# Optimization experiments

Hardware: AMD Instinct MI355X
Metric: run time of the kernel (lower is better)

## Reference

```python
import jax, jax.numpy as jnp
import numpy as np

TAU = 1.0
EPS = 1e-8
JITTER = 1e-6
W_OCC, W_ENT, W_COLLAPSE = 1.0, 0.0, 0.1


def fps_anchors_mu(mu, mask_bool, K):
    """Farthest-point sampling of K anchors from mu [B,N,3], mask_bool [B,N]."""
    B, N, _ = mu.shape
    barange = jnp.arange(B)
    cnt = jnp.maximum(mask_bool.sum(1, keepdims=True), 1)  # [B,1]
    mean = (mu * mask_bool[..., None]).sum(1, keepdims=True) / cnt[..., None]
    d2 = ((mu - mean) ** 2).sum(-1)
    d2 = jnp.where(mask_bool, d2, -1.0)
    first = jnp.argmax(d2, axis=-1)  # [B]
    last = mu[barange, first]  # [B,3]
    min_d2 = ((mu - last[:, None, :]) ** 2).sum(-1)
    min_d2 = jnp.where(mask_bool, min_d2, -1.0)

    def step(md2, _):
        sel = jnp.argmax(md2, axis=-1)  # [B]
        lm = mu[barange, sel]  # [B,3]
        nd2 = ((mu - lm[:, None, :]) ** 2).sum(-1)
        nd2 = jnp.where(mask_bool, nd2, -1.0)
        md2 = jnp.where(md2 == -1.0, nd2, jnp.minimum(md2, nd2))
        return md2, sel

    _, sels = jax.lax.scan(step, min_d2, None, length=K - 1)  # sels [K-1,B]
    idx = jnp.concatenate([first[:, None], sels.T], axis=1)  # [B,K]
    return jax.lax.stop_gradient(idx)


def merge_gaussians_soft(mu, Sigma, A):
    denom = jnp.maximum(A.sum(axis=1, keepdims=True), EPS)  # [B,1,K]
    w = A / denom  # [B,N,K]
    mu_c = jnp.einsum('bnk,bnd->bkd', w, mu)  # [B,K,3]
    intra = jnp.einsum('bnk,bnij->bkij', w, Sigma)  # [B,K,3,3]
    diff = mu[:, :, None, :] - mu_c[:, None, :, :]  # [B,N,K,3]
    inter = jnp.einsum('bnk,bnkd,bnke->bkde', w, diff, diff)
    Sigma_c = intra + inter
    Sigma_c = 0.5 * (Sigma_c + jnp.swapaxes(Sigma_c, -1, -2))
    Sigma_c = Sigma_c + JITTER * jnp.eye(3, dtype=Sigma_c.dtype)
    return mu_c, Sigma_c


def collapse_loss(A, mask):
    B, N, K = A.shape
    Am = A * mask[..., None]
    X = jnp.swapaxes(Am, 1, 2)  # [B,K,N]
    X = X / jnp.maximum(jnp.linalg.norm(X, axis=-1, keepdims=True), EPS)
    G = jnp.einsum('bkn,bln->bkl', X, X)
    eye = jnp.eye(K, dtype=A.dtype)[None]
    off = (G - eye) * (1.0 - eye)
    return jnp.mean(off ** 2)


def reference(s, mu, Sigma, mask, W_proj, slot_embed, log_sigma_mu, w_sem, w_mu):
    B, N, C = s.shape
    K = slot_embed.shape[0]
    mask_bool = mask > 0.5

    # semantic logits
    s_proj = jnp.einsum('bnc,dc->bnd', s, W_proj)  # Linear, no bias
    logits_sem = jnp.einsum('bnc,kc->bnk', s_proj, slot_embed) / max(TAU, 1e-6)

    # spatial logits from FPS anchors
    idx = fps_anchors_mu(mu, mask_bool, K)  # [B,K]
    mu_anchor = jnp.take_along_axis(mu, idx[..., None], axis=1)  # [B,K,3]
    dist2 = ((mu[:, :, None, :] - mu_anchor[:, None, :, :]) ** 2).sum(-1)  # [B,N,K]
    sigma2 = jnp.maximum(jnp.exp(log_sigma_mu), 1e-4) ** 2
    logits_mu = -dist2 / (2.0 * sigma2)

    logits = w_sem * logits_sem + w_mu * logits_mu
    logits = jnp.where(mask[..., None] < 0.5, -1e9, logits)
    A = jax.nn.softmax(logits, axis=-1) * mask[..., None]

    denom = jnp.maximum(A.sum(axis=1), 1e-8)  # [B,K]
    s_c = jnp.einsum('bnk,bnc->bkc', A, s) / denom[..., None]
    mu_c, Sigma_c = merge_gaussians_soft(mu, Sigma, A)

    # losses
    occ = A.sum(axis=1)
    occ = occ / jnp.maximum(occ.sum(axis=-1, keepdims=True), 1e-8)
    target = jnp.full_like(occ, 1.0 / max(K, 1))
    loss_occ = jnp.mean((occ - target) ** 2)
    Ac = jnp.maximum(A, 1e-8)
    ent = -(Ac * jnp.log(Ac)).sum(-1)
    ent = (ent * mask).sum() / jnp.maximum(mask.sum(), 1.0)
    loss_collapse = collapse_loss(A, mask)
    total = W_OCC * loss_occ + W_ENT * ent + W_COLLAPSE * loss_collapse
    return A, s_c, mu_c, Sigma_c, total


def setup_inputs() -> dict:
    key = jax.random.key(0)
    ks = jax.random.split(key, 8)
    B, N, C, K = 4, 8192, 128, 683
    s = jax.random.normal(ks[0], (B, N, C), dtype=jnp.float32)
    mu = jax.random.normal(ks[1], (B, N, 3), dtype=jnp.float32)
    Sig = jax.random.normal(ks[2], (B, N, 3, 3), dtype=jnp.float32)
    Sigma = 0.5 * (Sig + jnp.swapaxes(Sig, -1, -2))
    mask = jnp.ones((B, N), dtype=jnp.float32)
    W_proj = jax.random.normal(ks[3], (C, C), dtype=jnp.float32) / np.sqrt(C)
    slot_embed = jax.random.normal(ks[4], (K, C), dtype=jnp.float32) * 0.02
    log_sigma_mu = jnp.zeros((), dtype=jnp.float32)  # sigma_mu_init = 1.0
    w_sem = jnp.ones((), dtype=jnp.float32)
    w_mu = jnp.ones((), dtype=jnp.float32)
    return {"s": s, "mu": mu, "Sigma": Sigma, "mask": mask, "W_proj": W_proj,
            "slot_embed": slot_embed, "log_sigma_mu": log_sigma_mu,
            "w_sem": w_sem, "w_mu": w_mu}
```

## Files before the change

### kernel.cpp

```cpp
#include <hip/hip_runtime.h>
#include <hip/hip_bf16.h>
#include <math.h>

#define B_ 4
#define N_ 8192
#define C_ 128
#define K_ 683
#define KP_ 768
#define KT_ 704

#define WS_ET      0
#define WS_ANCH    98304
#define WS_EXT     110592
#define WS_EPART   634880
#define WS_MPART   1355776
#define WS_SUMA    2142208
#define WS_NORM    2145024
#define WS_LOSSP2  2147840
#define WS_ST      2147968
#define WS_AT      4245120
#define WS_NEW_END 16828032
#define OLD_PART   634880
#define OLD_SUMA   4419584
#define OLD_NORM   4422400
#define OLD_GPART  4425216
#define OLD_LOSSP  9143808

#define OUT_A      0
#define OUT_SC     22380544ULL
#define OUT_MUC    22730240ULL
#define OUT_SGC    22738436ULL
#define OUT_TOT    22763024ULL

typedef __attribute__((ext_vector_type(8))) short bf16x8s;
typedef __attribute__((ext_vector_type(4))) float f32x4;

static __device__ __forceinline__ unsigned short f2bf_rne(float f) {
  unsigned int u = __builtin_bit_cast(unsigned int, f);
  unsigned int r = (u + 0x7fffu + ((u >> 16) & 1u)) >> 16;
  return (unsigned short)r;
}

static __device__ __forceinline__ unsigned int f2ord(float f) {
  unsigned int u = __builtin_bit_cast(unsigned int, f);
  return (u & 0x80000000u) ? ~u : (u | 0x80000000u);
}

static __device__ __forceinline__ unsigned long long umax64(unsigned long long a,
                                                           unsigned long long b) {
  return a > b ? a : b;
}

__global__ __launch_bounds__(256) void build_ET_k(const float* __restrict__ Wp,
                                                  const float* __restrict__ se,
                                                  float* __restrict__ ET) {
  int idx = blockIdx.x * 256 + threadIdx.x;
  if (idx >= C_ * KP_) return;
  int c = idx / KP_;
  int k = idx % KP_;
  float acc = 0.f;
  if (k < K_) {
    for (int d = 0; d < C_; d++) acc = fmaf(se[k * C_ + d], Wp[d * C_ + c], acc);
  }
  ET[idx] = acc;
}

__global__ __launch_bounds__(512, 1) void fused_k(const float* __restrict__ s,
    const float* __restrict__ mu, const float* __restrict__ Sigma,
    const float* __restrict__ mask, const float* __restrict__ ET,
    float* __restrict__ anchors, float* __restrict__ ext,
    float* __restrict__ A, unsigned short* __restrict__ sT) {
  const int bid = blockIdx.x;
  const int tid = threadIdx.x;

  __shared__ __align__(16) float s_lds[32][132];
  __shared__ __align__(16) float et_lds[8][KP_];
  __shared__ __align__(16) float muL[N_ * 3];
  __shared__ __align__(16) float Tt[64][72];
  __shared__ double redd[8][4];
  __shared__ unsigned long long redk[2][8];
  __shared__ float an_s[4];

  if (bid >= 1092) {
    const int sb = bid - 1092;
    const int b = sb >> 6;
    const int rest = sb & 63;
    const int chalf = rest >> 5;
    const int ns = rest & 31;
    const int c0 = chalf * 64, n0 = ns * 256;
#pragma unroll
    for (int t2 = 0; t2 < 4; t2++) {
      const int nb = n0 + t2 * 64;
      {
        int n_loc = tid >> 3;
        int cb = (tid & 7) * 8;
        const float* sp = s + ((size_t)(b * N_ + nb + n_loc)) * C_ + c0 + cb;
        float4 v0 = *(const float4*)(sp);
        float4 v1 = *(const float4*)(sp + 4);
        Tt[cb + 0][n_loc] = v0.x; Tt[cb + 1][n_loc] = v0.y;
        Tt[cb + 2][n_loc] = v0.z; Tt[cb + 3][n_loc] = v0.w;
        Tt[cb + 4][n_loc] = v1.x; Tt[cb + 5][n_loc] = v1.y;
        Tt[cb + 6][n_loc] = v1.z; Tt[cb + 7][n_loc] = v1.w;
      }
      __syncthreads();
      {
        int row = tid >> 3;
        int qo = tid & 7;
        float4 f0 = *(const float4*)(&Tt[row][qo * 8]);
        float4 f1 = *(const float4*)(&Tt[row][qo * 8 + 4]);
        unsigned short o[8];
        o[0] = f2bf_rne(f0.x); o[1] = f2bf_rne(f0.y); o[2] = f2bf_rne(f0.z); o[3] = f2bf_rne(f0.w);
        o[4] = f2bf_rne(f1.x); o[5] = f2bf_rne(f1.y); o[6] = f2bf_rne(f1.z); o[7] = f2bf_rne(f1.w);
        unsigned short* dst = sT + ((size_t)(b * C_ + c0 + row)) * N_ + nb + qo * 8;
        *(uint4*)dst = *(uint4*)o;
      }
      __syncthreads();
    }
    return;
  }

  if (bid >= 1028) {
    int idx = (bid - 1028) * 512 + tid;
    if (idx < B_ * N_) {
      float x = mu[(size_t)idx * 3 + 0];
      float y = mu[(size_t)idx * 3 + 1];
      float z = mu[(size_t)idx * 3 + 2];
      const float* S = Sigma + (size_t)idx * 9;
      float* e = ext + (size_t)idx * 16;
      e[0] = x; e[1] = y; e[2] = z;
      e[3] = x * x; e[4] = x * y; e[5] = x * z;
      e[6] = y * y; e[7] = y * z; e[8] = z * z;
      e[9] = S[0]; e[10] = S[1]; e[11] = S[2]; e[12] = S[4]; e[13] = S[5]; e[14] = S[8];
      e[15] = 1.f;
    }
    return;
  }

  if (bid >= 4) {
    const int gb = bid - 4;
    const int b = gb >> 8;
    const int n0 = (gb & 255) * 32;
    const int nt = tid >> 6;
    const int kt = tid & 63;
    {
      const float* sb = s + ((size_t)(b * N_ + n0)) * C_;
      int r = tid >> 4;
      int cb = (tid & 15) * 8;
#pragma unroll
      for (int q = 0; q < 2; q++) {
        float4 v = *(const float4*)(sb + (size_t)r * C_ + cb + q * 4);
        *(float4*)(&s_lds[r][cb + q * 4]) = v;
      }
    }
    float acc[4][12];
#pragma unroll
    for (int i = 0; i < 4; i++)
#pragma unroll
      for (int j = 0; j < 12; j++) acc[i][j] = 0.f;

    for (int cc = 0; cc < 16; cc++) {
      __syncthreads();
#pragma unroll
      for (int q = 0; q < 3; q++) {
        int fid = q * 512 + tid;
        int cl = fid / 192;
        int o4 = fid % 192;
        *(float4*)(&et_lds[cl][o4 * 4]) = *(const float4*)(ET + (size_t)(cc * 8 + cl) * KP_ + o4 * 4);
      }
      __syncthreads();
#pragma unroll
      for (int c8 = 0; c8 < 8; c8++) {
        int c = cc * 8 + c8;
        float sv0 = s_lds[nt * 4 + 0][c];
        float sv1 = s_lds[nt * 4 + 1][c];
        float sv2 = s_lds[nt * 4 + 2][c];
        float sv3 = s_lds[nt * 4 + 3][c];
#pragma unroll
        for (int j = 0; j < 12; j++) {
          float ev = et_lds[c8][kt + 64 * j];
          acc[0][j] = fmaf(sv0, ev, acc[0][j]);
          acc[1][j] = fmaf(sv1, ev, acc[1][j]);
          acc[2][j] = fmaf(sv2, ev, acc[2][j]);
          acc[3][j] = fmaf(sv3, ev, acc[3][j]);
        }
      }
    }
#pragma unroll
    for (int i = 0; i < 4; i++) {
      float* Arow = A + ((size_t)(b * N_ + n0 + nt * 4 + i)) * K_;
#pragma unroll
      for (int j = 0; j < 12; j++) {
        int k = kt + 64 * j;
        if (k < K_) Arow[k] = acc[i][j];
      }
    }
    return;
  }

  const int b = bid;
  const int t = tid;
  const int wv = t >> 6;
  const float* mub = mu + (size_t)b * N_ * 3;
  const float* mkb = mask + (size_t)b * N_;
  float px[16], py[16], pz[16], md[16];

  double sx = 0, sy = 0, sz = 0, sc = 0;
#pragma unroll
  for (int i = 0; i < 16; i++) {
    int p = i * 512 + t;
    px[i] = mub[p * 3 + 0];
    py[i] = mub[p * 3 + 1];
    pz[i] = mub[p * 3 + 2];
    muL[p * 3 + 0] = px[i];
    muL[p * 3 + 1] = py[i];
    muL[p * 3 + 2] = pz[i];
    float mk = mkb[p];
    bool valid = (mk > 0.5f);
    md[i] = valid ? 3.4e38f : -1.f;
    if (valid) { sx += px[i]; sy += py[i]; sz += pz[i]; sc += 1.0; }
  }
  for (int off = 32; off; off >>= 1) {
    sx += __shfl_xor(sx, off);
    sy += __shfl_xor(sy, off);
    sz += __shfl_xor(sz, off);
    sc += __shfl_xor(sc, off);
  }
  if ((t & 63) == 0) { redd[wv][0] = sx; redd[wv][1] = sy; redd[wv][2] = sz; redd[wv][3] = sc; }
  __syncthreads();
  if (t == 0) {
    double ax0 = 0, ay0 = 0, az0 = 0, ac = 0;
    for (int w = 0; w < 8; w++) { ax0 += redd[w][0]; ay0 += redd[w][1]; az0 += redd[w][2]; ac += redd[w][3]; }
    if (ac < 1.0) ac = 1.0;
    an_s[0] = (float)(ax0 / ac); an_s[1] = (float)(ay0 / ac); an_s[2] = (float)(az0 / ac);
  }
  __syncthreads();

  float ax, ay, az;
  {
    float cx = an_s[0], cy = an_s[1], cz = an_s[2];
    float bv = -2.f, bv2 = -2.f;
    int bi = 0, bi2 = 0;
#pragma unroll
    for (int i = 0; i < 16; i++) {
      float dx = px[i] - cx, dy = py[i] - cy, dz = pz[i] - cz;
      float d2 = __fadd_rn(__fadd_rn(__fmul_rn(dx, dx), __fmul_rn(dy, dy)), __fmul_rn(dz, dz));
      float v = (md[i] < 0.f) ? -1.f : d2;
      int p = i * 512 + t;
      if (i & 1) { if (v > bv2) { bv2 = v; bi2 = p; } }
      else       { if (v > bv)  { bv = v;  bi = p; } }
    }
    if (bv2 > bv || (bv2 == bv && bi2 < bi)) { bv = bv2; bi = bi2; }
    unsigned long long k0 = ((unsigned long long)f2ord(bv) << 32) | (unsigned int)(~bi);
    for (int off = 32; off; off >>= 1) {
      unsigned long long ok = __shfl_xor(k0, off);
      if (ok > k0) k0 = ok;
    }
    if ((t & 63) == 0) redk[0][wv] = k0;
    __syncthreads();
    unsigned long long a0 = redk[0][0], a1 = redk[0][1], a2 = redk[0][2], a3 = redk[0][3];
    unsigned long long a4 = redk[0][4], a5 = redk[0][5], a6 = redk[0][6], a7 = redk[0][7];
    unsigned long long bk = umax64(umax64(umax64(a0, a1), umax64(a2, a3)),
                                  umax64(umax64(a4, a5), umax64(a6, a7)));
    int besti = (int)(~(unsigned int)bk);
    ax = muL[besti * 3 + 0]; ay = muL[besti * 3 + 1]; az = muL[besti * 3 + 2];
    if (t == 0) {
      float aa = ax * ax + ay * ay + az * az;
      float4 st = {ax, ay, az, aa};
      *(float4*)(anchors + ((size_t)b * KP_ + 0) * 4) = st;
    }
  }

  for (int k = 1; k < K_; k++) {
    const int par = k & 1;
    float bv = -2.f, bv2 = -2.f;
    int bi = 0, bi2 = 0;
#pragma unroll
    for (int i = 0; i < 16; i++) {
      float dx = px[i] - ax, dy = py[i] - ay, dz = pz[i] - az;
      float d2 = __fadd_rn(__fadd_rn(__fmul_rn(dx, dx), __fmul_rn(dy, dy)), __fmul_rn(dz, dz));
      float m = fminf(md[i], d2);
      md[i] = m;
      int p = i * 512 + t;
      if (i & 1) { if (m > bv2) { bv2 = m; bi2 = p; } }
      else       { if (m > bv)  { bv = m;  bi = p; } }
    }
    if (bv2 > bv || (bv2 == bv && bi2 < bi)) { bv = bv2; bi = bi2; }
    unsigned long long kk = ((unsigned long long)f2ord(bv) << 32) | (unsigned int)(~bi);
    for (int off = 32; off; off >>= 1) {
      unsigned long long ok = __shfl_xor(kk, off);
      if (ok > kk) kk = ok;
    }
    if ((t & 63) == 0) redk[par][wv] = kk;
    __syncthreads();
    unsigned long long a0 = redk[par][0], a1 = redk[par][1], a2 = redk[par][2], a3 = redk[par][3];
    unsigned long long a4 = redk[par][4], a5 = redk[par][5], a6 = redk[par][6], a7 = redk[par][7];
    unsigned long long bk = umax64(umax64(umax64(a0, a1), umax64(a2, a3)),
                                  umax64(umax64(a4, a5), umax64(a6, a7)));
    int besti = (int)(~(unsigned int)bk);
    ax = muL[besti * 3 + 0]; ay = muL[besti * 3 + 1]; az = muL[besti * 3 + 2];
    if (t == 0) {
      float aa = ax * ax + ay * ay + az * az;
      float4 st = {ax, ay, az, aa};
      *(float4*)(anchors + ((size_t)b * KP_ + k) * 4) = st;
    }
  }
  for (int k = K_ + t; k < KP_; k += 512) {
    float4 z4 = {0.f, 0.f, 0.f, 0.f};
    *(float4*)(anchors + ((size_t)b * KP_ + k) * 4) = z4;
  }
}

__global__ __launch_bounds__(256) void spatial_softmax_k(
    const float* __restrict__ mu, const float* __restrict__ mask,
    const float* __restrict__ anchors, const float* __restrict__ lsm_p,
    const float* __restrict__ wsem_p, const float* __restrict__ wmu_p,
    float* __restrict__ A) {
  const int bid = blockIdx.x;
  const int b = bid >> 11;
  const int n0 = (bid & 2047) * 4;
  const int tid = threadIdx.x;
  const int wv = tid >> 6;
  const int lane = tid & 63;
  __shared__ __align__(16) float anch_lds[KP_][4];
  for (int q = tid; q < KP_; q += 256)
    *(float4*)(&anch_lds[q][0]) = *(const float4*)(anchors + ((size_t)b * KP_ + q) * 4);
  __syncthreads();

  const float sg = fmaxf(expf(lsm_p[0]), 1e-4f);
  const float inv2s2 = 0.5f / (sg * sg);
  const float wsem = wsem_p[0];
  const float wmu = wmu_p[0];

  const size_t gr = (size_t)b * N_ + n0 + wv;
  const float* mp = mu + gr * 3;
  float x = mp[0], y = mp[1], z = mp[2];
  float mq = x * x + y * y + z * z;
  float mk = mask[gr];
  float* Arow = A + gr * K_;

  float v[11];
  float m = -3e38f;
#pragma unroll
  for (int j = 0; j < 11; j++) {
    int k = lane + 64 * j;
    if (k < K_) {
      float lsem = Arow[k];
      float4 a4 = *(const float4*)(&anch_lds[k][0]);
      float tdot = x * a4.x + y * a4.y + z * a4.z;
      float d2 = mq - 2.f * tdot + a4.w;
      float l = wsem * lsem - wmu * d2 * inv2s2;
      if (mk < 0.5f) l = -1e9f;
      v[j] = l;
    } else v[j] = -1e30f;
    m = fmaxf(m, v[j]);
  }
  for (int off = 32; off; off >>= 1) m = fmaxf(m, __shfl_xor(m, off));
  float sum = 0.f;
#pragma unroll
  for (int j = 0; j < 11; j++) { float e = expf(v[j] - m); v[j] = e; sum += e; }
  for (int off = 32; off; off >>= 1) sum += __shfl_xor(sum, off);
  float r = mk / sum;
#pragma unroll
  for (int j = 0; j < 11; j++) {
    int k = lane + 64 * j;
    if (k < K_) Arow[k] = v[j] * r;
  }
}

__global__ __launch_bounds__(256) void transpose_at_k(const float* __restrict__ A,
    unsigned short* __restrict__ At) {
  const int bid = blockIdx.x;
  const int ntile = bid % 128;
  const int rem = bid / 128;
  const int kt = rem % 12;
  const int b = rem / 12;
  const int k0 = kt * 64, n0 = ntile * 64;
  const int tid = threadIdx.x;
  __shared__ __align__(16) unsigned short T[64][72];

  {
    const int n_loc = tid >> 4;
    const int k4 = (tid & 15) * 4;
#pragma unroll
    for (int nn = 0; nn < 4; nn++) {
      int n = n_loc + 16 * nn;
      const float* ar = A + ((size_t)(b * N_ + n0 + n)) * K_;
#pragma unroll
      for (int q = 0; q < 4; q++) {
        int kk = k0 + k4 + q;
        float f = (kk < K_) ? ar[kk] : 0.f;
        T[k4 + q][n] = f2bf_rne(f);
      }
    }
  }
  __syncthreads();
  {
    const int k_loc = tid >> 2;
    const int c = tid & 3;
    uint4 v0 = *(const uint4*)(&T[k_loc][c * 16]);
    uint4 v1 = *(const uint4*)(&T[k_loc][c * 16 + 8]);
    unsigned short* dst = At + ((size_t)(b * KP_ + k0 + k_loc)) * N_ + n0 + c * 16;
    *(uint4*)dst = v0;
    *(uint4*)(dst + 8) = v1;
  }
}

__global__ __launch_bounds__(256) void gemm2_mfma_k(const unsigned short* __restrict__ At,
    const unsigned short* __restrict__ sT, float* __restrict__ mpart) {
  const int bid = blockIdx.x;
  const int np = bid / 24;
  const int rem = bid % 24;
  const int b = rem / 6;
  const int kt2 = rem % 6;
  const int k0 = kt2 * 128;
  const int tid = threadIdx.x;
  const int l = tid & 63;
  const int w = tid >> 6;
  const int wr = w >> 1, wc = w & 1;

  __shared__ __align__(16) unsigned short Ak_lds[128 * 72];
  __shared__ __align__(16) unsigned short Bc_lds[128 * 72];

  f32x4 acc[4][4];
#pragma unroll
  for (int i = 0; i < 4; i++)
#pragma unroll
    for (int j = 0; j < 4; j++) acc[i][j] = (f32x4){0.f, 0.f, 0.f, 0.f};

  const unsigned short* gk = At + ((size_t)(b * KP_ + k0)) * N_;
  const unsigned short* gc = sT + ((size_t)(b * C_)) * N_;
  const int nbase = np * 4096;

  for (int ch = 0; ch < 64; ch++) {
    const int n0 = nbase + ch * 64;
    __syncthreads();
#pragma unroll
    for (int q = 0; q < 4; q++) {
      int chunk = tid + 256 * q;
      int row = chunk >> 3, slot = chunk & 7;
      uint4 v = *(const uint4*)(gk + (size_t)row * N_ + n0 + slot * 8);
      *(uint4*)(Ak_lds + row * 72 + slot * 8) = v;
      uint4 v2 = *(const uint4*)(gc + (size_t)row * N_ + n0 + slot * 8);
      *(uint4*)(Bc_lds + row * 72 + slot * 8) = v2;
    }
    __syncthreads();
#pragma unroll
    for (int ks = 0; ks < 2; ks++) {
      const int noff = (l >> 4) * 8 + ks * 32;
      bf16x8s af[4], bfr[4];
#pragma unroll
      for (int f = 0; f < 4; f++) {
        af[f]  = *(const bf16x8s*)(Ak_lds + (wr * 64 + f * 16 + (l & 15)) * 72 + noff);
        bfr[f] = *(const bf16x8s*)(Bc_lds + (wc * 64 + f * 16 + (l & 15)) * 72 + noff);
      }
#pragma unroll
      for (int i = 0; i < 4; i++)
#pragma unroll
        for (int j = 0; j < 4; j++)
          acc[i][j] = __builtin_amdgcn_mfma_f32_16x16x32_bf16(af[i], bfr[j], acc[i][j], 0, 0, 0);
    }
  }
  float* mp = mpart + ((size_t)((np * 4 + b) * KP_ + k0)) * C_;
#pragma unroll
  for (int i = 0; i < 4; i++) {
#pragma unroll
    for (int j = 0; j < 4; j++) {
#pragma unroll
      for (int r = 0; r < 4; r++) {
        int ki = wr * 64 + i * 16 + (l >> 4) * 4 + r;
        int ci = wc * 64 + j * 16 + (l & 15);
        mp[(size_t)ki * C_ + ci] = acc[i][j][r];
      }
    }
  }
}

__global__ __launch_bounds__(256) void gemm2_ext_k(const float* __restrict__ A,
    const float* __restrict__ ext, float* __restrict__ epart) {
  const int bid = blockIdx.x;
  const int np = bid / 44;
  const int rem = bid % 44;
  const int b = rem / 11;
  const int k0 = (rem % 11) * 64;
  const int n0 = np * 1024;
  const int tid = threadIdx.x;
  const int kt = tid & 15;
  const int ft = tid >> 4;
  __shared__ __align__(16) float A_lds[32][64];
  __shared__ __align__(16) float F_lds[32][32];
  float acc[4][2];
#pragma unroll
  for (int c = 0; c < 4; c++) { acc[c][0] = 0.f; acc[c][1] = 0.f; }
  float asq[4] = {0.f, 0.f, 0.f, 0.f};

  for (int ch = 0; ch < 32; ch++) {
    int nb = n0 + ch * 32;
    __syncthreads();
#pragma unroll
    for (int p = 0; p < 8; p++) {
      int q = tid + 256 * p; int r = q >> 6; int c = q & 63; int k = k0 + c;
      A_lds[r][c] = (k < K_) ? A[((size_t)(b * N_ + nb + r)) * K_ + k] : 0.f;
    }
#pragma unroll
    for (int p = 0; p < 2; p++) {
      int q = tid + 256 * p; int r = q >> 4; int e = q & 15;
      F_lds[r][e] = ext[((size_t)(b * N_ + nb + r)) * 16 + e];
      F_lds[r][16 + e] = 0.f;
    }
    __syncthreads();
#pragma unroll
    for (int i = 0; i < 32; i++) {
      float a0 = A_lds[i][kt * 4 + 0];
      float a1 = A_lds[i][kt * 4 + 1];
      float a2 = A_lds[i][kt * 4 + 2];
      float a3 = A_lds[i][kt * 4 + 3];
      if (ft == 0) {
        asq[0] = fmaf(a0, a0, asq[0]); asq[1] = fmaf(a1, a1, asq[1]);
        asq[2] = fmaf(a2, a2, asq[2]); asq[3] = fmaf(a3, a3, asq[3]);
      }
#pragma unroll
      for (int f = 0; f < 2; f++) {
        float fv = F_lds[i][ft * 2 + f];
        acc[0][f] = fmaf(a0, fv, acc[0][f]);
        acc[1][f] = fmaf(a1, fv, acc[1][f]);
        acc[2][f] = fmaf(a2, fv, acc[2][f]);
        acc[3][f] = fmaf(a3, fv, acc[3][f]);
      }
    }
  }
#pragma unroll
  for (int c = 0; c < 4; c++) {
    size_t base = ((size_t)((np * 4 + b) * KT_ + k0 + kt * 4 + c)) * 32;
#pragma unroll
    for (int f = 0; f < 2; f++) {
      int fidx = ft * 2 + f;
      if (fidx < 16) epart[base + fidx] = acc[c][f];
    }
    if (ft == 0) epart[base + 16] = asq[c];
  }
}

__global__ __launch_bounds__(256) void postproc2_k(const float* __restrict__ mpart,
    const float* __restrict__ epart, float* __restrict__ out,
    float* __restrict__ sumA_ws, float* __restrict__ norm_ws) {
  const int gw = blockIdx.x * 4 + (threadIdx.x >> 6);
  const int lane = threadIdx.x & 63;
  const int b = gw / K_;
  const int k = gw % K_;
  float v0 = 0.f, v1 = 0.f, v2 = 0.f, v3 = 0.f;
#pragma unroll
  for (int np = 0; np < 2; np++) {
    const float* r = mpart + ((size_t)((np * 4 + b) * KP_ + k)) * C_;
    v0 += r[lane];
    v1 += r[64 + lane];
  }
#pragma unroll
  for (int np = 0; np < 8; np++) {
    const float* e = epart + ((size_t)((np * 4 + b) * KT_ + k)) * 32;
    if (lane < 16) v2 += e[lane];
    if (lane == 0) v3 += e[16];
  }
  float sumA = __shfl(v2, 15);
  float asq = __shfl(v3, 0);
  float denom = fmaxf(sumA, 1e-8f);
  float inv = 1.f / denom;
  out[OUT_SC + ((size_t)(b * K_ + k)) * C_ + lane] = v0 * inv;
  out[OUT_SC + ((size_t)(b * K_ + k)) * C_ + 64 + lane] = v1 * inv;
  float m0 = __shfl(v2, 0) * inv;
  float m1 = __shfl(v2, 1) * inv;
  float m2 = __shfl(v2, 2) * inv;
  if (lane < 3) out[OUT_MUC + ((size_t)(b * K_ + k)) * 3 + lane] = (lane == 0) ? m0 : ((lane == 1) ? m1 : m2);
  float W = sumA * inv;
  float fac = 2.f - W;
  float M2s[6], Sgs[6];
#pragma unroll
  for (int j = 0; j < 6; j++) { M2s[j] = __shfl(v2, 3 + j); Sgs[j] = __shfl(v2, 9 + j); }
  if (lane < 9) {
    int d = lane / 3, e = lane % 3;
    int lo = min(d, e), hi = max(d, e);
    int j = hi + 2 * lo - ((lo * (lo - 1)) >> 1);
    float mud = (d == 0) ? m0 : ((d == 1) ? m1 : m2);
    float mue = (e == 0) ? m0 : ((e == 1) ? m1 : m2);
    float M2j = (j == 0) ? M2s[0] : (j == 1) ? M2s[1] : (j == 2) ? M2s[2] : (j == 3) ? M2s[3] : (j == 4) ? M2s[4] : M2s[5];
    float Sgj = (j == 0) ? Sgs[0] : (j == 1) ? Sgs[1] : (j == 2) ? Sgs[2] : (j == 3) ? Sgs[3] : (j == 4) ? Sgs[4] : Sgs[5];
    float val = (Sgj + M2j) * inv - mud * mue * fac;
    if (d == e) val += 1e-6f;
    out[OUT_SGC + ((size_t)(b * K_ + k)) * 9 + lane] = val;
  }
  if (lane == 0) { sumA_ws[b * KT_ + k] = sumA; norm_ws[b * KT_ + k] = sqrtf(asq); }
}

__global__ __launch_bounds__(256) void gram_mfma_k(const unsigned short* __restrict__ At,
    const float* __restrict__ norm_ws, float* __restrict__ lossp) {
  const int bid = blockIdx.x;
  const int b = bid / 21;
  int p = bid % 21;
  int tk = 0, tl = 0;
  { int pp = p; for (int r0 = 0; r0 < 6; r0++) { int cnt = 6 - r0; if (pp < cnt) { tk = r0; tl = r0 + pp; break; } pp -= cnt; } }
  const int k0 = tk * 128, l0 = tl * 128;
  const int tid = threadIdx.x;
  const int l = tid & 63;
  const int w = tid >> 6;
  const int wr = w >> 1, wc = w & 1;

  __shared__ __align__(16) unsigned short Ak_lds[128 * 72];
  __shared__ __align__(16) unsigned short Al_lds[128 * 72];
  __shared__ float nk_s[128], nl_s[128], red_s[4];

  if (tid < 128) {
    int kk = k0 + tid;
    nk_s[tid] = (kk < K_) ? fmaxf(norm_ws[b * KT_ + kk], 1e-8f) : 1.f;
  } else {
    int ll2 = l0 + tid - 128;
    nl_s[tid - 128] = (ll2 < K_) ? fmaxf(norm_ws[b * KT_ + ll2], 1e-8f) : 1.f;
  }

  f32x4 acc[4][4];
#pragma unroll
  for (int i = 0; i < 4; i++)
#pragma unroll
    for (int j = 0; j < 4; j++) acc[i][j] = (f32x4){0.f, 0.f, 0.f, 0.f};

  const unsigned short* gk = At + ((size_t)(b * KP_ + k0)) * N_;
  const unsigned short* gl = At + ((size_t)(b * KP_ + l0)) * N_;

  for (int ch = 0; ch < 128; ch++) {
    const int n0 = ch * 64;
    __syncthreads();
#pragma unroll
    for (int q = 0; q < 4; q++) {
      int chunk = tid + 256 * q;
      int row = chunk >> 3, slot = chunk & 7;
      uint4 v = *(const uint4*)(gk + (size_t)row * N_ + n0 + slot * 8);
      *(uint4*)(Ak_lds + row * 72 + slot * 8) = v;
      uint4 v2 = *(const uint4*)(gl + (size_t)row * N_ + n0 + slot * 8);
      *(uint4*)(Al_lds + row * 72 + slot * 8) = v2;
    }
    __syncthreads();
#pragma unroll
    for (int ks = 0; ks < 2; ks++) {
      const int noff = (l >> 4) * 8 + ks * 32;
      bf16x8s af[4], bfr[4];
#pragma unroll
      for (int f = 0; f < 4; f++) {
        af[f]  = *(const bf16x8s*)(Ak_lds + (wr * 64 + f * 16 + (l & 15)) * 72 + noff);
        bfr[f] = *(const bf16x8s*)(Al_lds + (wc * 64 + f * 16 + (l & 15)) * 72 + noff);
      }
#pragma unroll
      for (int i = 0; i < 4; i++)
#pragma unroll
        for (int j = 0; j < 4; j++)
          acc[i][j] = __builtin_amdgcn_mfma_f32_16x16x32_bf16(af[i], bfr[j], acc[i][j], 0, 0, 0);
    }
  }

  float local = 0.f;
  const float wgt = (tk == tl) ? 1.f : 2.f;
#pragma unroll
  for (int i = 0; i < 4; i++) {
#pragma unroll
    for (int j = 0; j < 4; j++) {
#pragma unroll
      for (int r = 0; r < 4; r++) {
        int ki = wr * 64 + i * 16 + (l >> 4) * 4 + r;
        int li = wc * 64 + j * 16 + (l & 15);
        int gkk = k0 + ki, gll = l0 + li;
        if (gkk < K_ && gll < K_ && gkk != gll) {
          float g = acc[i][j][r];
          float x = g / (nk_s[ki] * nl_s[li]);
          local = fmaf(wgt * x, x, local);
        }
      }
    }
  }
  for (int off = 32; off; off >>= 1) local += __shfl_xor(local, off);
  if ((tid & 63) == 0) red_s[w] = local;
  __syncthreads();
  if (tid == 0) lossp[bid] = red_s[0] + red_s[1] + red_s[2] + red_s[3];
}

__global__ __launch_bounds__(256) void final2_k(const float* __restrict__ sumA_ws,
    const float* __restrict__ lossp, float* __restrict__ out) {
  const int lane = threadIdx.x & 63;
  const int wv = threadIdx.x >> 6;
  __shared__ float occ_s[4];
  __shared__ float col_s[4];
  float sb = 0.f;
  for (int k = lane; k < K_; k += 64) sb += sumA_ws[wv * KT_ + k];
  for (int off = 32; off; off >>= 1) sb += __shfl_xor(sb, off);
  float Sb = fmaxf(sb, 1e-8f);
  float lo = 0.f;
  const float tgt = 1.f / (float)K_;
  for (int k = lane; k < K_; k += 64) {
    float o = sumA_ws[wv * KT_ + k] / Sb - tgt;
    lo = fmaf(o, o, lo);
  }
  for (int off = 32; off; off >>= 1) lo += __shfl_xor(lo, off);
  if (lane == 0) occ_s[wv] = lo;
  float c = 0.f;
  for (int i = threadIdx.x; i < 84; i += 256) c += lossp[i];
  for (int off = 32; off; off >>= 1) c += __shfl_xor(c, off);
  if (lane == 0) col_s[wv] = c;
  __syncthreads();
  if (threadIdx.x == 0) {
    float loss_occ = (occ_s[0] + occ_s[1] + occ_s[2] + occ_s[3]) / (float)(B_ * K_);
    float coll = (col_s[0] + col_s[1] + col_s[2] + col_s[3]) / ((float)B_ * K_ * K_);
    out[OUT_TOT] = loss_occ + 0.1f * coll;
  }
}

__global__ __launch_bounds__(256) void gemm2_k(const float* __restrict__ A,
    const float* __restrict__ s, const float* __restrict__ ext,
    float* __restrict__ part) {
  const int bid = blockIdx.x;
  const int np = bid / 44;
  const int rem = bid % 44;
  const int b = rem / 11;
  const int k0 = (rem % 11) * 64;
  const int n0 = np * 1024;
  const int tid = threadIdx.x;
  const int kt = tid & 15;
  const int ft = tid >> 4;
  __shared__ __align__(16) float A_lds[32][64];
  __shared__ __align__(16) float F_lds[32][160];
  float acc[4][10];
#pragma unroll
  for (int c = 0; c < 4; c++)
#pragma unroll
    for (int f = 0; f < 10; f++) acc[c][f] = 0.f;
  float asq[4] = {0.f, 0.f, 0.f, 0.f};
  for (int ch = 0; ch < 32; ch++) {
    int nb = n0 + ch * 32;
    __syncthreads();
#pragma unroll
    for (int p = 0; p < 8; p++) {
      int q = tid + 256 * p; int r = q >> 6; int c = q & 63; int k = k0 + c;
      A_lds[r][c] = (k < K_) ? A[((size_t)(b * N_ + nb + r)) * K_ + k] : 0.f;
    }
#pragma unroll
    for (int p = 0; p < 16; p++) {
      int q = tid + 256 * p; int r = q >> 7; int c = q & 127;
      F_lds[r][c] = s[((size_t)(b * N_ + nb + r)) * C_ + c];
    }
#pragma unroll
    for (int p = 0; p < 2; p++) {
      int q = tid + 256 * p; int r = q >> 4; int e = q & 15;
      F_lds[r][128 + e] = ext[((size_t)(b * N_ + nb + r)) * 16 + e];
      F_lds[r][144 + e] = 0.f;
    }
    __syncthreads();
#pragma unroll
    for (int i = 0; i < 32; i++) {
      float a0 = A_lds[i][kt * 4 + 0];
      float a1 = A_lds[i][kt * 4 + 1];
      float a2 = A_lds[i][kt * 4 + 2];
      float a3 = A_lds[i][kt * 4 + 3];
      if (ft == 0) {
        asq[0] = fmaf(a0, a0, asq[0]); asq[1] = fmaf(a1, a1, asq[1]);
        asq[2] = fmaf(a2, a2, asq[2]); asq[3] = fmaf(a3, a3, asq[3]);
      }
#pragma unroll
      for (int f = 0; f < 10; f++) {
        float fv = F_lds[i][ft * 10 + f];
        acc[0][f] = fmaf(a0, fv, acc[0][f]);
        acc[1][f] = fmaf(a1, fv, acc[1][f]);
        acc[2][f] = fmaf(a2, fv, acc[2][f]);
        acc[3][f] = fmaf(a3, fv, acc[3][f]);
      }
    }
  }
#pragma unroll
  for (int c = 0; c < 4; c++) {
    size_t base = ((size_t)((np * 4 + b) * KT_ + k0 + kt * 4 + c)) * 168;
#pragma unroll
    for (int f = 0; f < 10; f++) part[base + ft * 10 + f] = acc[c][f];
    if (ft == 0) part[base + 160] = asq[c];
  }
}

__global__ __launch_bounds__(256) void postproc_k(const float* __restrict__ part,
    float* __restrict__ out, float* __restrict__ sumA_ws, float* __restrict__ norm_ws) {
  const int gw = blockIdx.x * 4 + (threadIdx.x >> 6);
  const int lane = threadIdx.x & 63;
  const int b = gw / K_;
  const int k = gw % K_;
  float v0 = 0.f, v1 = 0.f, v2 = 0.f, v3 = 0.f;
  for (int np = 0; np < 8; np++) {
    const float* r = part + ((size_t)((np * 4 + b) * KT_ + k)) * 168;
    v0 += r[lane];
    v1 += r[64 + lane];
    if (lane < 16) v2 += r[128 + lane];
    if (lane == 0) v3 += r[160];
  }
  float sumA = __shfl(v2, 15);
  float asq = __shfl(v3, 0);
  float denom = fmaxf(sumA, 1e-8f);
  float inv = 1.f / denom;
  out[OUT_SC + ((size_t)(b * K_ + k)) * C_ + lane] = v0 * inv;
  out[OUT_SC + ((size_t)(b * K_ + k)) * C_ + 64 + lane] = v1 * inv;
  float m0 = __shfl(v2, 0) * inv;
  float m1 = __shfl(v2, 1) * inv;
  float m2 = __shfl(v2, 2) * inv;
  if (lane < 3) out[OUT_MUC + ((size_t)(b * K_ + k)) * 3 + lane] = (lane == 0) ? m0 : ((lane == 1) ? m1 : m2);
  float W = sumA * inv;
  float fac = 2.f - W;
  float M2s[6], Sgs[6];
#pragma unroll
  for (int j = 0; j < 6; j++) { M2s[j] = __shfl(v2, 3 + j); Sgs[j] = __shfl(v2, 9 + j); }
  if (lane < 9) {
    int d = lane / 3, e = lane % 3;
    int lo = min(d, e), hi = max(d, e);
    int j = hi + 2 * lo - ((lo * (lo - 1)) >> 1);
    float mud = (d == 0) ? m0 : ((d == 1) ? m1 : m2);
    float mue = (e == 0) ? m0 : ((e == 1) ? m1 : m2);
    float M2j = (j == 0) ? M2s[0] : (j == 1) ? M2s[1] : (j == 2) ? M2s[2] : (j == 3) ? M2s[3] : (j == 4) ? M2s[4] : M2s[5];
    float Sgj = (j == 0) ? Sgs[0] : (j == 1) ? Sgs[1] : (j == 2) ? Sgs[2] : (j == 3) ? Sgs[3] : (j == 4) ? Sgs[4] : Sgs[5];
    float val = (Sgj + M2j) * inv - mud * mue * fac;
    if (d == e) val += 1e-6f;
    out[OUT_SGC + ((size_t)(b * K_ + k)) * 9 + lane] = val;
  }
  if (lane == 0) { sumA_ws[b * KT_ + k] = sumA; norm_ws[b * KT_ + k] = sqrtf(asq); }
}

__device__ __forceinline__ int swz(int f) { return f ^ (((f >> 5) & 3) << 3); }

__global__ __launch_bounds__(256) void gram_k(const float* __restrict__ A,
                                              float* __restrict__ Gpart) {
  const int bid = blockIdx.x;
  const int np = bid & 1;
  int q = bid >> 1;
  const int b = q / 21;
  int p = q % 21;
  int tk = 0, tl = 0;
  { int pp = p; for (int r0 = 0; r0 < 6; r0++) { int cnt = 6 - r0; if (pp < cnt) { tk = r0; tl = r0 + pp; break; } pp -= cnt; } }
  const int k0 = tk * 128, l0 = tl * 128;
  const int n0 = np * 4096;
  const int tid = threadIdx.x;
  const int ktid = tid & 15, ltid = tid >> 4;
  const bool diag = (tk == tl);
  __shared__ __align__(16) float Ak[32][128];
  __shared__ __align__(16) float Al[32][128];
  float acc[8][8];
#pragma unroll
  for (int i = 0; i < 8; i++)
#pragma unroll
    for (int j = 0; j < 8; j++) acc[i][j] = 0.f;
  const int kb = swz(ktid * 8);
  const int lb = swz(ltid * 8);
  for (int ch = 0; ch < 128; ch++) {
    int nb = n0 + ch * 32;
    __syncthreads();
#pragma unroll
    for (int pq = 0; pq < 16; pq++) {
      int qq = tid + 256 * pq; int r = qq >> 7; int c = qq & 127;
      int kk = k0 + c;
      Ak[r][swz(c)] = (kk < K_) ? A[((size_t)(b * N_ + nb + r)) * K_ + kk] : 0.f;
      if (!diag) {
        int ll = l0 + c;
        Al[r][swz(c)] = (ll < K_) ? A[((size_t)(b * N_ + nb + r)) * K_ + ll] : 0.f;
      }
    }
    __syncthreads();
    const float (*Alp)[128] = diag ? Ak : Al;
#pragma unroll
    for (int i = 0; i < 32; i++) {
      float4 ka = *(const float4*)(&Ak[i][kb]);
      float4 kb4 = *(const float4*)(&Ak[i][kb + 4]);
      float4 la = *(const float4*)(&Alp[i][lb]);
      float4 lb4 = *(const float4*)(&Alp[i][lb + 4]);
      float av[8] = {ka.x, ka.y, ka.z, ka.w, kb4.x, kb4.y, kb4.z, kb4.w};
      float lv[8] = {la.x, la.y, la.z, la.w, lb4.x, lb4.y, lb4.z, lb4.w};
#pragma unroll
      for (int ii = 0; ii < 8; ii++)
#pragma unroll
        for (int jj = 0; jj < 8; jj++)
          acc[ii][jj] = fmaf(av[ii], lv[jj], acc[ii][jj]);
    }
  }
#pragma unroll
  for (int ii = 0; ii < 8; ii++) {
    int kk = k0 + ktid * 8 + ii;
    float* gp = Gpart + ((size_t)((np * 4 + b) * KP_ + kk)) * KP_ + l0 + ltid * 8;
#pragma unroll
    for (int jj = 0; jj < 8; jj++) gp[jj] = acc[ii][jj];
  }
}

__global__ __launch_bounds__(256) void loss_part_k(const float* __restrict__ Gpart,
    const float* __restrict__ norm_ws, float* __restrict__ lossp) {
  const long long total = (long long)B_ * 21 * 16384;
  float local = 0.f;
  for (long long idx = (long long)blockIdx.x * 256 + threadIdx.x; idx < total; idx += (long long)512 * 256) {
    int e = (int)(idx & 16383);
    int rest = (int)(idx >> 14);
    int p = rest % 21;
    int b = rest / 21;
    int tk = 0, tl = 0;
    { int pp = p; for (int r0 = 0; r0 < 6; r0++) { int cnt = 6 - r0; if (pp < cnt) { tk = r0; tl = r0 + pp; break; } pp -= cnt; } }
    int i = e >> 7, j = e & 127;
    int k = tk * 128 + i, l = tl * 128 + j;
    if (k < K_ && l < K_ && k != l) {
      size_t i0 = ((size_t)((0 * 4 + b) * KP_ + k)) * KP_ + l;
      size_t i1 = ((size_t)((1 * 4 + b) * KP_ + k)) * KP_ + l;
      float g = Gpart[i0] + Gpart[i1];
      float nk = fmaxf(norm_ws[b * KT_ + k], 1e-8f);
      float nl2 = fmaxf(norm_ws[b * KT_ + l], 1e-8f);
      float x = g / (nk * nl2);
      float wgt = (tk == tl) ? 1.f : 2.f;
      local = fmaf(wgt * x, x, local);
    }
  }
  __shared__ float red[4];
  for (int off = 32; off; off >>= 1) local += __shfl_xor(local, off);
  if ((threadIdx.x & 63) == 0) red[threadIdx.x >> 6] = local;
  __syncthreads();
  if (threadIdx.x == 0) lossp[blockIdx.x] = red[0] + red[1] + red[2] + red[3];
}

__global__ __launch_bounds__(256) void final_k(const float* __restrict__ sumA_ws,
    const float* __restrict__ lossp, float* __restrict__ out) {
  const int lane = threadIdx.x & 63;
  const int wv = threadIdx.x >> 6;
  __shared__ float occ_s[4];
  __shared__ float col_s[4];
  float sb = 0.f;
  for (int k = lane; k < K_; k += 64) sb += sumA_ws[wv * KT_ + k];
  for (int off = 32; off; off >>= 1) sb += __shfl_xor(sb, off);
  float Sb = fmaxf(sb, 1e-8f);
  float lo = 0.f;
  const float tgt = 1.f / (float)K_;
  for (int k = lane; k < K_; k += 64) {
    float o = sumA_ws[wv * KT_ + k] / Sb - tgt;
    lo = fmaf(o, o, lo);
  }
  for (int off = 32; off; off >>= 1) lo += __shfl_xor(lo, off);
  if (lane == 0) occ_s[wv] = lo;
  float c = lossp[threadIdx.x] + lossp[threadIdx.x + 256];
  for (int off = 32; off; off >>= 1) c += __shfl_xor(c, off);
  if (lane == 0) col_s[wv] = c;
  __syncthreads();
  if (threadIdx.x == 0) {
    float loss_occ = (occ_s[0] + occ_s[1] + occ_s[2] + occ_s[3]) / (float)(B_ * K_);
    float coll = (col_s[0] + col_s[1] + col_s[2] + col_s[3]) / ((float)B_ * K_ * K_);
    out[OUT_TOT] = loss_occ + 0.1f * coll;
  }
}

extern "C" void kernel_launch(void* const* d_in, const int* in_sizes, int n_in,
                              void* d_out, int out_size, void* d_ws, size_t ws_size,
                              hipStream_t stream) {
  const float* s = (const float*)d_in[0];
  const float* mu = (const float*)d_in[1];
  const float* Sigma = (const float*)d_in[2];
  const float* mask = (const float*)d_in[3];
  const float* Wp = (const float*)d_in[4];
  const float* se = (const float*)d_in[5];
  const float* lsm = (const float*)d_in[6];
  const float* wsem = (const float*)d_in[7];
  const float* wmu = (const float*)d_in[8];
  float* out = (float*)d_out;
  float* ws = (float*)d_ws;

  float* ET = ws + WS_ET;
  float* anch = ws + WS_ANCH;
  float* ext = ws + WS_EXT;

  const bool use_mfma = ws_size >= (size_t)WS_NEW_END * 4;

  if (use_mfma) {
    float* epart = ws + WS_EPART;
    float* mpart = ws + WS_MPART;
    float* sumA = ws + WS_SUMA;
    float* nrm = ws + WS_NORM;
    float* lossp2 = ws + WS_LOSSP2;
    unsigned short* sT = (unsigned short*)(ws + WS_ST);
    unsigned short* At = (unsigned short*)(ws + WS_AT);

    hipLaunchKernelGGL(build_ET_k, dim3(384), dim3(256), 0, stream, Wp, se, ET);
    hipLaunchKernelGGL(fused_k, dim3(1348), dim3(512), 0, stream, s, mu, Sigma, mask, ET, anch, ext, out, sT);
    hipLaunchKernelGGL(spatial_softmax_k, dim3(8192), dim3(256), 0, stream, mu, mask, anch, lsm, wsem, wmu, out);
    hipLaunchKernelGGL(transpose_at_k, dim3(4 * 12 * 128), dim3(256), 0, stream, out, At);
    hipLaunchKernelGGL(gemm2_mfma_k, dim3(48), dim3(256), 0, stream, At, sT, mpart);
    hipLaunchKernelGGL(gemm2_ext_k, dim3(352), dim3(256), 0, stream, out, ext, epart);
    hipLaunchKernelGGL(postproc2_k, dim3(683), dim3(256), 0, stream, mpart, epart, out, sumA, nrm);
    hipLaunchKernelGGL(gram_mfma_k, dim3(84), dim3(256), 0, stream, At, nrm, lossp2);
    hipLaunchKernelGGL(final2_k, dim3(1), dim3(256), 0, stream, sumA, lossp2, out);
  } else {
    float* part = ws + OLD_PART;
    float* sumA = ws + OLD_SUMA;
    float* nrm = ws + OLD_NORM;
    float* Gpart = ws + OLD_GPART;
    float* lossp = ws + OLD_LOSSP;
    unsigned short* sT = (unsigned short*)(ws + WS_ST);

    hipLaunchKernelGGL(build_ET_k, dim3(384), dim3(256), 0, stream, Wp, se, ET);
    hipLaunchKernelGGL(fused_k, dim3(1348), dim3(512), 0, stream, s, mu, Sigma, mask, ET, anch, ext, out, sT);
    hipLaunchKernelGGL(spatial_softmax_k, dim3(8192), dim3(256), 0, stream, mu, mask, anch, lsm, wsem, wmu, out);
    hipLaunchKernelGGL(gemm2_k, dim3(352), dim3(256), 0, stream, out, s, ext, part);
    hipLaunchKernelGGL(postproc_k, dim3(683), dim3(256), 0, stream, part, out, sumA, nrm);
    hipLaunchKernelGGL(gram_k, dim3(168), dim3(256), 0, stream, out, Gpart);
    hipLaunchKernelGGL(loss_part_k, dim3(512), dim3(256), 0, stream, Gpart, nrm, lossp);
    hipLaunchKernelGGL(final_k, dim3(1), dim3(256), 0, stream, sumA, lossp, out);
  }
}
```

Measured before the change: 1.264 ms.

## Fuse spatial softmax with bf16 transpose of assignment matrix into one kernel

Merges the spatial softmax kernel and the separate transpose/bf16-convert kernel into a single kernel. Each block handles 32 rows, computes the softmax, writes A in fp32, packs bf16 values into an LDS tile, and writes the transposed At directly. This avoids re-reading the full A matrix from global memory for the transpose and removes one launch. In exchange, blocks use more LDS and the grid shrinks from 8192 to 1024 blocks, which may lower occupancy.

```diff
diff --git a/kernel.cpp b/kernel.cpp
--- a/kernel.cpp
+++ b/kernel.cpp
@@ -310,6 +310,90 @@
   }
 }
 
+__global__ __launch_bounds__(256) void postA_k(
+    const float* __restrict__ mu, const float* __restrict__ mask,
+    const float* __restrict__ anchors, const float* __restrict__ lsm_p,
+    const float* __restrict__ wsem_p, const float* __restrict__ wmu_p,
+    float* __restrict__ A, unsigned short* __restrict__ At) {
+  const int bid = blockIdx.x;
+  const int b = bid >> 8;
+  const int n0 = (bid & 255) * 32;
+  const int tid = threadIdx.x;
+  const int wv = tid >> 6;
+  const int lane = tid & 63;
+  __shared__ __align__(16) float anch_lds[KP_][4];
+  __shared__ __align__(16) unsigned short T[KP_][40];
+
+  for (int q = tid; q < KP_; q += 256)
+    *(float4*)(&anch_lds[q][0]) = *(const float4*)(anchors + ((size_t)b * KP_ + q) * 4);
+  __syncthreads();
+
+  const float sg = fmaxf(expf(lsm_p[0]), 1e-4f);
+  const float inv2s2 = 0.5f / (sg * sg);
+  const float wsem = wsem_p[0];
+  const float wmu = wmu_p[0];
+
+#pragma unroll
+  for (int g = 0; g < 2; g++) {
+    const int r0 = wv * 8 + g * 4;
+    unsigned short tpack[12][4];
+#pragma unroll
+    for (int rr = 0; rr < 4; rr++) {
+      const size_t gr = (size_t)b * N_ + n0 + r0 + rr;
+      const float* mp = mu + gr * 3;
+      float x = mp[0], y = mp[1], z = mp[2];
+      float mq = x * x + y * y + z * z;
+      float mk = mask[gr];
+      float* Arow = A + gr * K_;
+
+      float v[11];
+      float m = -3e38f;
+#pragma unroll
+      for (int j = 0; j < 11; j++) {
+        int k = lane + 64 * j;
+        if (k < K_) {
+          float lsem = Arow[k];
+          float4 a4 = *(const float4*)(&anch_lds[k][0]);
+          float tdot = x * a4.x + y * a4.y + z * a4.z;
+          float d2 = mq - 2.f * tdot + a4.w;
+          float l = wsem * lsem - wmu * d2 * inv2s2;
+          if (mk < 0.5f) l = -1e9f;
+          v[j] = l;
+        } else v[j] = -1e30f;
+        m = fmaxf(m, v[j]);
+      }
+      for (int off = 32; off; off >>= 1) m = fmaxf(m, __shfl_xor(m, off));
+      float sum = 0.f;
+#pragma unroll
+      for (int j = 0; j < 11; j++) { float e = expf(v[j] - m); v[j] = e; sum += e; }
+      for (int off = 32; off; off >>= 1) sum += __shfl_xor(sum, off);
+      float r = mk / sum;
+#pragma unroll
+      for (int j = 0; j < 11; j++) {
+        int k = lane + 64 * j;
+        float av = v[j] * r;
+        if (k < K_) { Arow[k] = av; tpack[j][rr] = f2bf_rne(av); }
+        else tpack[j][rr] = 0;
+      }
+      tpack[11][rr] = 0;
+    }
+#pragma unroll
+    for (int j = 0; j < 12; j++) {
+      int k = lane + 64 * j;
+      *(unsigned long long*)(&T[k][r0]) = *(const unsigned long long*)(&tpack[j][0]);
+    }
+  }
+  __syncthreads();
+#pragma unroll
+  for (int kq = 0; kq < 3; kq++) {
+    int k = tid + 256 * kq;
+    const uint4* src = (const uint4*)(&T[k][0]);
+    unsigned short* dst = At + ((size_t)(b * KP_ + k)) * N_ + n0;
+#pragma unroll
+    for (int q = 0; q < 4; q++) *(uint4*)(dst + q * 8) = src[q];
+  }
+}
+
 __global__ __launch_bounds__(256) void spatial_softmax_k(
     const float* __restrict__ mu, const float* __restrict__ mask,
     const float* __restrict__ anchors, const float* __restrict__ lsm_p,
@@ -364,44 +448,6 @@
   for (int j = 0; j < 11; j++) {
     int k = lane + 64 * j;
     if (k < K_) Arow[k] = v[j] * r;
-  }
-}
-
-__global__ __launch_bounds__(256) void transpose_at_k(const float* __restrict__ A,
-    unsigned short* __restrict__ At) {
-  const int bid = blockIdx.x;
-  const int ntile = bid % 128;
-  const int rem = bid / 128;
-  const int kt = rem % 12;
-  const int b = rem / 12;
-  const int k0 = kt * 64, n0 = ntile * 64;
-  const int tid = threadIdx.x;
-  __shared__ __align__(16) unsigned short T[64][72];
-
-  {
-    const int n_loc = tid >> 4;
-    const int k4 = (tid & 15) * 4;
-#pragma unroll
-    for (int nn = 0; nn < 4; nn++) {
-      int n = n_loc + 16 * nn;
-      const float* ar = A + ((size_t)(b * N_ + n0 + n)) * K_;
-#pragma unroll
-      for (int q = 0; q < 4; q++) {
-        int kk = k0 + k4 + q;
-        float f = (kk < K_) ? ar[kk] : 0.f;
-        T[k4 + q][n] = f2bf_rne(f);
-      }
-    }
-  }
-  __syncthreads();
-  {
-    const int k_loc = tid >> 2;
-    const int c = tid & 3;
-    uint4 v0 = *(const uint4*)(&T[k_loc][c * 16]);
-    uint4 v1 = *(const uint4*)(&T[k_loc][c * 16 + 8]);
-    unsigned short* dst = At + ((size_t)(b * KP_ + k0 + k_loc)) * N_ + n0 + c * 16;
-    *(uint4*)dst = v0;
-    *(uint4*)(dst + 8) = v1;
   }
 }
 
@@ -978,8 +1024,7 @@
 
     hipLaunchKernelGGL(build_ET_k, dim3(384), dim3(256), 0, stream, Wp, se, ET);
     hipLaunchKernelGGL(fused_k, dim3(1348), dim3(512), 0, stream, s, mu, Sigma, mask, ET, anch, ext, out, sT);
-    hipLaunchKernelGGL(spatial_softmax_k, dim3(8192), dim3(256), 0, stream, mu, mask, anch, lsm, wsem, wmu, out);
-    hipLaunchKernelGGL(transpose_at_k, dim3(4 * 12 * 128), dim3(256), 0, stream, out, At);
+    hipLaunchKernelGGL(postA_k, dim3(1024), dim3(256), 0, stream, mu, mask, anch, lsm, wsem, wmu, out, At);
     hipLaunchKernelGGL(gemm2_mfma_k, dim3(48), dim3(256), 0, stream, At, sT, mpart);
     hipLaunchKernelGGL(gemm2_ext_k, dim3(352), dim3(256), 0, stream, out, ext, epart);
     hipLaunchKernelGGL(postproc2_k, dim3(683), dim3(256), 0, stream, mpart, epart, out, sumA, nrm);
```

Result: no change. 1.253 ms (-0.9%).
